# Performance work log

Measured on AMD Instinct MI355X. Metric: run time of the kernel, lower is better.

Reference implementation:

```python
import jax, jax.numpy as jnp
import numpy as np

B, S, H, W, C = 16, 32, 84, 84, 4
HID, NH, L, A = 256, 4, 2, 18
HD = HID // NH
THETA = 10000.0
EPS = 1e-6


def _ln(x, s, b):
    m = jnp.mean(x, axis=-1, keepdims=True)
    v = jnp.mean(jnp.square(x - m), axis=-1, keepdims=True)
    return (x - m) / jnp.sqrt(v + EPS) * s + b


def _conv(x, w):
    return jax.lax.conv_general_dilated(x, w, (1, 1), 'SAME', dimension_numbers=('NHWC', 'HWIO', 'NHWC'))


def _rotate_half(x):
    xe = x[..., ::2]
    xo = x[..., 1::2]
    return jnp.stack((-xo, xe), axis=-1).reshape(x.shape)


def _rope(q, k):
    d = q.shape[-1]
    pos = jnp.arange(q.shape[-2], dtype=jnp.float32)
    inv_freq = 1.0 / jnp.asarray(THETA, jnp.float32) ** (jnp.arange(0, d, 2, dtype=jnp.float32) / d)
    ang = pos[:, None] * inv_freq[None, :]
    sin = jnp.repeat(jnp.sin(ang), 2, axis=-1)[None, None].astype(q.dtype)
    cos = jnp.repeat(jnp.cos(ang), 2, axis=-1)[None, None].astype(q.dtype)
    return q * cos + _rotate_half(q) * sin, k * cos + _rotate_half(k) * sin


def setup_inputs() -> dict:
    key = jax.random.key(0)
    ks = jax.random.split(key, 20)
    he = lambda k, shp, fan: jax.random.normal(k, shp, jnp.float32) * np.sqrt(2.0 / fan)
    return {
        'x': jax.random.normal(ks[0], (B, S, H, W, C), jnp.float32),
        'attention_padding': jnp.ones((B, S), jnp.bool_),
        'conv0_w': he(ks[1], (3, 3, C, 32), 3 * 3 * C),
        'conv0_b': jnp.zeros((32,), jnp.float32),
        'ln_c0_s': jnp.ones((32,), jnp.float32), 'ln_c0_b': jnp.zeros((32,), jnp.float32),
        'conv1_w': he(ks[2], (3, 3, 32, 64), 3 * 3 * 32),
        'conv1_b': jnp.zeros((64,), jnp.float32),
        'ln_c1_s': jnp.ones((64,), jnp.float32), 'ln_c1_b': jnp.zeros((64,), jnp.float32),
        'proj_w': he(ks[3], (64, HID), 64), 'proj_b': jnp.zeros((HID,), jnp.float32),
        'ln_p_s': jnp.ones((HID,), jnp.float32), 'ln_p_b': jnp.zeros((HID,), jnp.float32),
        'attn_qkv_w': he(ks[4], (L, HID, 3 * HID), HID),
        'attn_qkv_b': jnp.zeros((L, 3 * HID), jnp.float32),
        'attn_out_w': he(ks[5], (L, HID, HID), HID),
        'attn_out_b': jnp.zeros((L, HID), jnp.float32),
        'ln_a_s': jnp.ones((L, HID), jnp.float32), 'ln_a_b': jnp.zeros((L, HID), jnp.float32),
        'up_w': he(ks[6], (L, HID, 2 * HID), HID),
        'down_w': he(ks[7], (L, 2 * HID, HID), 2 * HID),
        'ln_m_s': jnp.ones((L, HID), jnp.float32), 'ln_m_b': jnp.zeros((L, HID), jnp.float32),
        'head_w': he(ks[8], (HID, A), HID), 'head_b': jnp.zeros((A,), jnp.float32),
    }


def reference(x, attention_padding, conv0_w, conv0_b, ln_c0_s, ln_c0_b, conv1_w, conv1_b,
              ln_c1_s, ln_c1_b, proj_w, proj_b, ln_p_s, ln_p_b, attn_qkv_w, attn_qkv_b,
              attn_out_w, attn_out_b, ln_a_s, ln_a_b, up_w, down_w, ln_m_s, ln_m_b,
              head_w, head_b):
    b, s = x.shape[:2]
    # CNN feature extractor over flattened (B*S) frames
    h = x.reshape(b * s, *x.shape[2:])
    h = jax.nn.relu(_ln(_conv(h, conv0_w) + conv0_b, ln_c0_s, ln_c0_b))
    h = jax.nn.relu(_ln(_conv(h, conv1_w) + conv1_b, ln_c1_s, ln_c1_b))
    h = jnp.mean(h, axis=(1, 2)).reshape(b, s, -1)  # (B,S,64)
    h = _ln(h @ proj_w + proj_b, ln_p_s, ln_p_b)    # (B,S,HID)
    pad = attention_padding
    causal = jnp.tril(jnp.ones((s, s), jnp.bool_))
    mask = pad[:, None, None, :] & causal[None, None]
    scale = jnp.asarray(HD, h.dtype) ** (-0.5)
    neg = jnp.asarray(-1e9, h.dtype)
    for i in range(L):
        r = h
        qkv = h @ attn_qkv_w[i] + attn_qkv_b[i]
        q, k, v = jnp.split(qkv, 3, axis=-1)
        sh = lambda t: t.reshape(b, s, NH, HD).transpose(0, 2, 1, 3)
        q, k, v = sh(q), sh(k), sh(v)
        q, k = _rope(q, k)
        logits = jnp.einsum('bhqd,bhkd->bhqk', q, k) * scale
        attn = jax.nn.softmax(jnp.where(mask, logits, neg), axis=-1)
        y = jnp.einsum('bhqk,bhkd->bhqd', attn, v).transpose(0, 2, 1, 3).reshape(b, s, HID)
        y = (y @ attn_out_w[i] + attn_out_b[i]) * pad[:, :, None].astype(h.dtype)
        h = _ln(y, ln_a_s[i], ln_a_b[i]) + r
        r = h
        u = jax.nn.relu(h @ up_w[i])
        h = _ln(u @ down_w[i], ln_m_s[i], ln_m_b[i]) + r
    return h @ head_w + head_b  # (B,S,action_dim)
```

## Files before the change

kernel.cpp:

```cpp
#include <hip/hip_runtime.h>
#include <hip/hip_bf16.h>

#define LN_EPS 1e-6f

typedef __attribute__((ext_vector_type(8))) short bf16x8;
typedef __attribute__((ext_vector_type(4))) float fx4;

struct U8 { union { bf16x8 v; uint2 p[2]; }; };

__device__ __forceinline__ unsigned short f2bf(float f) {
    union { __hip_bfloat16 b; unsigned short u; } cv;
    cv.b = __float2bfloat16(f);
    return cv.u;
}

__global__ void k_pad(const unsigned char* __restrict__ p, float* __restrict__ padf) {
    __shared__ int cnt;
    int t = threadIdx.x;
    if (t == 0) cnt = 0;
    __syncthreads();
    if (p[t]) atomicAdd(&cnt, 1);
    __syncthreads();
    float v;
    if (cnt > 256) v = p[t] ? 1.f : 0.f;
    else           v = ((const int*)p)[t] ? 1.f : 0.f;
    padf[t] = v;
}

__global__ void k_wprep(const float* __restrict__ w1, const float* __restrict__ w0,
                        unsigned short* __restrict__ wtb) {
    int idx = blockIdx.x * 256 + threadIdx.x;
    if (idx < 18432) {
        int j  = idx & 7;
        int kg = (idx >> 3) & 3;
        int co = (idx >> 5) & 63;
        int tp = idx >> 11;
        wtb[idx] = f2bf(w1[((size_t)tp * 32 + kg * 8 + j) * 64 + co]);
    } else {
        int r = idx - 18432;
        int ch = r >> 6, k = r & 63;
        float v = 0.f;
        if (k < 36) v = w0[(size_t)k * 32 + ch];
        wtb[idx] = f2bf(v);
    }
}

__global__ void k_wpack(const float* __restrict__ qkvw, const float* __restrict__ ow,
                        const float* __restrict__ upw, const float* __restrict__ dww,
                        const float* __restrict__ pw, unsigned short* __restrict__ wpk)
{
    int idx = blockIdx.x * 256 + threadIdx.x;
    if (idx >= 1064960) return;
    float v;
    if (idx < 393216) {
        int l = idx / 196608, rm = idx % 196608, n = rm >> 8, k = rm & 255;
        v = qkvw[((size_t)l * 256 + k) * 768 + n];
    } else if (idx < 524288) {
        int r = idx - 393216, l = r >> 16, rm = r & 65535, n = rm >> 8, k = rm & 255;
        v = ow[((size_t)l * 256 + k) * 256 + n];
    } else if (idx < 786432) {
        int r = idx - 524288, l = r >> 17, rm = r & 131071, n = rm >> 8, k = rm & 255;
        v = upw[((size_t)l * 256 + k) * 512 + n];
    } else if (idx < 1048576) {
        int r = idx - 786432, l = r >> 17, rm = r & 131071, n = rm >> 9, k = rm & 511;
        v = dww[((size_t)l * 512 + k) * 256 + n];
    } else {
        int r = idx - 1048576, n = r >> 6, k = r & 63;
        v = pw[k * 256 + n];
    }
    wpk[idx] = f2bf(v);
}

__global__ __launch_bounds__(256, 3) void k_conv1(
    const float* __restrict__ x, const unsigned short* __restrict__ wtb,
    const float* __restrict__ c0b, const float* __restrict__ l0s, const float* __restrict__ l0b,
    const float* __restrict__ bias, const float* __restrict__ lns, const float* __restrict__ lnb,
    float* __restrict__ pooled)
{
    __shared__ __align__(16) unsigned short At[4][5][86][8];
    __shared__ __align__(16) unsigned short xs[7][86][4];
    __shared__ float pool_w[4][64];
    const int tid = threadIdx.x;
    const int img = blockIdx.x / 28;
    const int rg  = blockIdx.x - img * 28;
    const int y0  = rg * 3;

    const int lane = tid & 63;
    const int wv = tid >> 6;
    const int lo = lane & 15;
    const int kg = lane >> 4;

    if (tid >= 64 && tid < 104) {
        int z = tid - 64;
        int zk = z / 10, rem = z - zk * 10, zr = rem >> 1, side = rem & 1;
        *reinterpret_cast<uint4*>(&At[zk][zr][side ? 85 : 0][0]) = (uint4){0, 0, 0, 0};
    }
    if (tid >= 104 && tid < 118) {
        int z = tid - 104, row = z >> 1, side = z & 1;
        *reinterpret_cast<uint2*>(&xs[row][side ? 85 : 0][0]) = (uint2){0, 0};
    }
    for (int i = tid; i < 588; i += 256) {
        int row = i / 84, c = i - row * 84;
        int gy = y0 - 2 + row;
        float4 v = (float4){0.f, 0.f, 0.f, 0.f};
        if (gy >= 0 && gy < 84)
            v = *reinterpret_cast<const float4*>(x + ((size_t)img * 7056 + gy * 84 + c) * 4);
        unsigned l32 = (unsigned)f2bf(v.x) | ((unsigned)f2bf(v.y) << 16);
        unsigned h32 = (unsigned)f2bf(v.z) | ((unsigned)f2bf(v.w) << 16);
        *reinterpret_cast<uint2*>(&xs[row][c + 1][0]) = (uint2){l32, h32};
    }
    __syncthreads();

    {
        const unsigned short* wc0 = wtb + 18432;
        bf16x8 W0[2], W1[2];
        #pragma unroll
        for (int m = 0; m < 2; ++m) {
            W0[m] = *reinterpret_cast<const bf16x8*>(wc0 + (m * 16 + lo) * 64 + kg * 8);
            W1[m] = *reinterpret_cast<const bf16x8*>(wc0 + (m * 16 + lo) * 64 + 32 + kg * 8);
        }
        float cb[2][4], sg[2][4], bg[2][4];
        #pragma unroll
        for (int m = 0; m < 2; ++m)
            #pragma unroll
            for (int r = 0; r < 4; ++r) {
                int c = m * 16 + kg * 4 + r;
                cb[m][r] = c0b[c]; sg[m][r] = l0s[c]; bg[m][r] = l0b[c];
            }
        const int t0 = 2 * kg, t1 = 2 * kg + 1;
        const int dy0 = t0 / 3, dx0 = t0 % 3, dy1 = t1 / 3, dx1 = t1 % 3;
        const unsigned short* xsb = &xs[0][0][0];

        for (int it = 0; it < 7; ++it) {
            int np = it * 4 + wv;
            if (np >= 27) break;
            int px = np * 16 + lo;
            int pxc = px < 420 ? px : 419;
            int r5 = pxc / 84, col = pxc - r5 * 84;
            U8 a0u, a1u;
            a0u.p[0] = *reinterpret_cast<const uint2*>(xsb + ((r5 + dy0) * 86 + col + dx0) * 4);
            a0u.p[1] = *reinterpret_cast<const uint2*>(xsb + ((r5 + dy1) * 86 + col + dx1) * 4);
            if (kg == 0)
                a1u.p[0] = *reinterpret_cast<const uint2*>(xsb + ((r5 + 2) * 86 + col + 2) * 4);
            else
                a1u.p[0] = (uint2){0, 0};
            a1u.p[1] = (uint2){0, 0};

            fx4 c2[2];
            c2[0] = (fx4){0.f, 0.f, 0.f, 0.f};
            c2[1] = (fx4){0.f, 0.f, 0.f, 0.f};
            c2[0] = __builtin_amdgcn_mfma_f32_16x16x32_bf16(W0[0], a0u.v, c2[0], 0, 0, 0);
            c2[0] = __builtin_amdgcn_mfma_f32_16x16x32_bf16(W1[0], a1u.v, c2[0], 0, 0, 0);
            c2[1] = __builtin_amdgcn_mfma_f32_16x16x32_bf16(W0[1], a0u.v, c2[1], 0, 0, 0);
            c2[1] = __builtin_amdgcn_mfma_f32_16x16x32_bf16(W1[1], a1u.v, c2[1], 0, 0, 0);

            float v[2][4], s = 0.f, q = 0.f;
            #pragma unroll
            for (int m = 0; m < 2; ++m)
                #pragma unroll
                for (int r = 0; r < 4; ++r) {
                    v[m][r] = c2[m][r] + cb[m][r];
                    s += v[m][r]; q += v[m][r] * v[m][r];
                }
            s += __shfl_xor(s, 16); q += __shfl_xor(q, 16);
            s += __shfl_xor(s, 32); q += __shfl_xor(q, 32);
            float mn = s * (1.f / 32.f);
            float inv = rsqrtf(q * (1.f / 32.f) - mn * mn + LN_EPS);

            if (px < 420) {
                int yA = y0 - 1 + r5;
                bool gv = (unsigned)yA < 84u;
                #pragma unroll
                for (int m = 0; m < 2; ++m) {
                    uint2 pk = (uint2){0, 0};
                    if (gv) {
                        unsigned short o0 = f2bf(fmaxf((v[m][0] - mn) * inv * sg[m][0] + bg[m][0], 0.f));
                        unsigned short o1 = f2bf(fmaxf((v[m][1] - mn) * inv * sg[m][1] + bg[m][1], 0.f));
                        unsigned short o2 = f2bf(fmaxf((v[m][2] - mn) * inv * sg[m][2] + bg[m][2], 0.f));
                        unsigned short o3 = f2bf(fmaxf((v[m][3] - mn) * inv * sg[m][3] + bg[m][3], 0.f));
                        pk.x = (unsigned)o0 | ((unsigned)o1 << 16);
                        pk.y = (unsigned)o2 | ((unsigned)o3 << 16);
                    }
                    *reinterpret_cast<uint2*>(&At[2 * m + (kg >> 1)][r5][col + 1][(kg & 1) * 4]) = pk;
                }
            }
        }
    }
    __syncthreads();

    int abase[4];
    #pragma unroll
    for (int m = 0; m < 4; ++m) {
        int pl = wv * 64 + m * 16 + lo;
        if (pl > 251) pl = 251;
        int rl = pl / 84;
        int c = pl - rl * 84;
        abase[m] = ((kg * 5 + rl) * 86 + c) * 8;
    }

    fx4 acc[4][4];
    #pragma unroll
    for (int m = 0; m < 4; ++m)
        #pragma unroll
        for (int n = 0; n < 4; ++n) acc[m][n] = (fx4){0.f, 0.f, 0.f, 0.f};

    const unsigned short* Abase = &At[0][0][0][0];
    #pragma unroll
    for (int dy = 0; dy < 3; ++dy) {
        #pragma unroll
        for (int dx = 0; dx < 3; ++dx) {
            const int t = dy * 3 + dx;
            bf16x8 Bf[4];
            #pragma unroll
            for (int n = 0; n < 4; ++n)
                Bf[n] = *reinterpret_cast<const bf16x8*>(
                    wtb + (size_t)((t * 64 + n * 16 + lo) * 4 + kg) * 8);
            #pragma unroll
            for (int m = 0; m < 4; ++m) {
                bf16x8 Af = *reinterpret_cast<const bf16x8*>(Abase + abase[m] + (dy * 86 + dx) * 8);
                #pragma unroll
                for (int n = 0; n < 4; ++n)
                    acc[m][n] = __builtin_amdgcn_mfma_f32_16x16x32_bf16(Af, Bf[n], acc[m][n], 0, 0, 0);
            }
        }
    }

    float bs[4], ss[4], bb[4];
    #pragma unroll
    for (int n = 0; n < 4; ++n) {
        int c = n * 16 + lo;
        bs[n] = bias[c]; ss[n] = lns[c]; bb[n] = lnb[c];
    }
    float pv[4] = {0.f, 0.f, 0.f, 0.f};
    #pragma unroll
    for (int m = 0; m < 4; ++m) {
        #pragma unroll
        for (int r = 0; r < 4; ++r) {
            float v0 = acc[m][0][r] + bs[0], v1 = acc[m][1][r] + bs[1];
            float v2 = acc[m][2][r] + bs[2], v3 = acc[m][3][r] + bs[3];
            float s = v0 + v1 + v2 + v3;
            float q = v0 * v0 + v1 * v1 + v2 * v2 + v3 * v3;
            #pragma unroll
            for (int off = 1; off < 16; off <<= 1) {
                s += __shfl_xor(s, off);
                q += __shfl_xor(q, off);
            }
            float mn = s * (1.f / 64.f);
            float var = q * (1.f / 64.f) - mn * mn;
            float inv = rsqrtf(var + LN_EPS);
            int pix = wv * 64 + m * 16 + kg * 4 + r;
            float valid = (pix < 252) ? 1.f : 0.f;
            pv[0] += fmaxf((v0 - mn) * inv * ss[0] + bb[0], 0.f) * valid;
            pv[1] += fmaxf((v1 - mn) * inv * ss[1] + bb[1], 0.f) * valid;
            pv[2] += fmaxf((v2 - mn) * inv * ss[2] + bb[2], 0.f) * valid;
            pv[3] += fmaxf((v3 - mn) * inv * ss[3] + bb[3], 0.f) * valid;
        }
    }
    #pragma unroll
    for (int n = 0; n < 4; ++n) {
        float v = pv[n];
        v += __shfl_xor(v, 16);
        v += __shfl_xor(v, 32);
        if (lane < 16) pool_w[wv][n * 16 + lane] = v;
    }
    __syncthreads();
    if (tid < 64) {
        float s = pool_w[0][tid] + pool_w[1][tid] + pool_w[2][tid] + pool_w[3][tid];
        atomicAdd(&pooled[img * 64 + tid], s);
    }
}

template<int MT, int NT, int KS>
__device__ __forceinline__ void mfma_gemm(
    const unsigned short* A, int lda, int m0,
    const unsigned short* B, int ldb, int nt0,
    fx4 (&acc)[MT][NT], int lane)
{
    const int lo = lane & 15, kg = lane >> 4;
    #pragma unroll
    for (int ks = 0; ks < KS; ++ks) {
        const int k = ks * 32 + kg * 8;
        bf16x8 af[MT];
        #pragma unroll
        for (int m = 0; m < MT; ++m)
            af[m] = *reinterpret_cast<const bf16x8*>(A + (size_t)((m0 + m) * 16 + lo) * lda + k);
        #pragma unroll
        for (int n = 0; n < NT; ++n) {
            bf16x8 bf = *reinterpret_cast<const bf16x8*>(B + (size_t)((nt0 + n) * 16 + lo) * ldb + k);
            #pragma unroll
            for (int m = 0; m < MT; ++m)
                acc[m][n] = __builtin_amdgcn_mfma_f32_16x16x32_bf16(af[m], bf, acc[m][n], 0, 0, 0);
        }
    }
}

__device__ __forceinline__ void ln_update(
    const float* outs , float* hs, unsigned short* hs_b,
    const float* gs, const float* gb, bool resid, int w, int lane)
{
    #pragma unroll
    for (int i = 0; i < 4; ++i) {
        int r = w * 4 + i;
        float x[4], s = 0.f, q = 0.f;
        #pragma unroll
        for (int j = 0; j < 4; ++j) {
            x[j] = outs[r * 257 + lane + 64 * j];
            s += x[j]; q += x[j] * x[j];
        }
        #pragma unroll
        for (int off = 1; off < 64; off <<= 1) {
            s += __shfl_xor(s, off);
            q += __shfl_xor(q, off);
        }
        float mn = s * (1.f / 256.f);
        float inv = rsqrtf(q * (1.f / 256.f) - mn * mn + LN_EPS);
        #pragma unroll
        for (int j = 0; j < 4; ++j) {
            int c = lane + 64 * j;
            float nv = (x[j] - mn) * inv * gs[c] + gb[c];
            if (resid) nv += hs[r * 256 + c];
            hs[r * 256 + c] = nv;
            hs_b[r * 264 + c] = f2bf(nv);
        }
    }
}

__global__ __launch_bounds__(512) void k_xformer(
    const float* __restrict__ pooled, const float* __restrict__ padf,
    const unsigned short* __restrict__ wpk,
    const float* __restrict__ pb, const float* __restrict__ lps, const float* __restrict__ lpb,
    const float* __restrict__ qkvb, const float* __restrict__ obv,
    const float* __restrict__ las, const float* __restrict__ lab,
    const float* __restrict__ lms, const float* __restrict__ lmb,
    const float* __restrict__ hw, const float* __restrict__ hb,
    float* __restrict__ out)
{
    __shared__ __align__(16) char smem[124032];
    float* hs = (float*)(smem);
    unsigned short* hs_b = (unsigned short*)(smem + 32768);
    unsigned short* R1 = (unsigned short*)(smem + 49664);
    unsigned short* q_s = R1;
    unsigned short* k_s = R1 + 9216;
    unsigned short* us_b = R1;
    unsigned short* v_cm = (unsigned short*)(smem + 86528);
    unsigned short* ys_b = (unsigned short*)(smem + 107008);
    float* outs = (float*)(smem + 86528);
    unsigned short* pool_b = (unsigned short*)(smem + 86528);
    float* padc = (float*)(smem + 123904);

    const int b = blockIdx.x, t = threadIdx.x;
    const int w = t >> 6, lane = t & 63, lo = lane & 15, kg = lane >> 4;

    if (t < 32) padc[t] = padf[b * 32 + t];
    for (int i = t; i < 2048; i += 512) {
        int r = i >> 6, k = i & 63;
        pool_b[r * 72 + k] = f2bf(pooled[((size_t)b * 32 + r) * 64 + k] * (1.f / 7056.f));
    }
    __syncthreads();

    {
        fx4 acc[1][4];
        #pragma unroll
        for (int n = 0; n < 4; ++n) acc[0][n] = (fx4){0.f, 0.f, 0.f, 0.f};
        int m0 = w & 1, nt0 = (w >> 1) * 4;
        mfma_gemm<1, 4, 2>(pool_b, 72, m0, wpk + 1048576, 64, nt0, acc, lane);
        __syncthreads();
        #pragma unroll
        for (int n = 0; n < 4; ++n) {
            int c = (nt0 + n) * 16 + lo;
            float bias = pb[c];
            #pragma unroll
            for (int rg = 0; rg < 4; ++rg)
                outs[(m0 * 16 + kg * 4 + rg) * 257 + c] = acc[0][n][rg] + bias;
        }
        __syncthreads();
        ln_update(outs, hs, hs_b, lps, lpb, false, w, lane);
        __syncthreads();
    }

    for (int l = 0; l < 2; ++l) {
        const unsigned short* wq = wpk + (size_t)l * 196608;
        const unsigned short* wo = wpk + 393216 + (size_t)l * 65536;
        const unsigned short* wu = wpk + 524288 + (size_t)l * 131072;
        const unsigned short* wd = wpk + 786432 + (size_t)l * 131072;

        {
            fx4 acc[2][6];
            #pragma unroll
            for (int m = 0; m < 2; ++m)
                #pragma unroll
                for (int n = 0; n < 6; ++n) acc[m][n] = (fx4){0.f, 0.f, 0.f, 0.f};
            int nt0 = w * 6;
            mfma_gemm<2, 6, 8>(hs_b, 264, 0, wq, 256, nt0, acc, lane);
            #pragma unroll
            for (int n = 0; n < 6; ++n) {
                int c = (nt0 + n) * 16 + lo;
                int kind = c >> 8, cl = c & 255, h = cl >> 6, d = cl & 63;
                float bias = qkvb[l * 768 + c];
                if (kind < 2) {
                    int j = d >> 1;
                    float freq = exp2f(-(float)j * 0.41524101186f);
                    unsigned short* dst = (kind ? k_s : q_s) + h * 2304;
                    #pragma unroll
                    for (int m = 0; m < 2; ++m)
                        #pragma unroll
                        for (int rg = 0; rg < 4; ++rg) {
                            float val = acc[m][n][rg] + bias;
                            float prt = __shfl_xor(val, 1);
                            int r = m * 16 + kg * 4 + rg;
                            float sn, cs;
                            __sincosf((float)r * freq, &sn, &cs);
                            float rv = (d & 1) ? (val * cs + prt * sn) : (val * cs - prt * sn);
                            dst[r * 72 + d] = f2bf(rv);
                        }
                } else {
                    #pragma unroll
                    for (int m = 0; m < 2; ++m)
                        #pragma unroll
                        for (int rg = 0; rg < 4; ++rg) {
                            int r = m * 16 + kg * 4 + rg;
                            v_cm[(h * 64 + d) * 40 + r] = f2bf(acc[m][n][rg] + bias);
                        }
                }
            }
            __syncthreads();
        }

        {
            int h = w >> 1, mt = w & 1;
            fx4 sc[1][2];
            sc[0][0] = (fx4){0.f, 0.f, 0.f, 0.f};
            sc[0][1] = (fx4){0.f, 0.f, 0.f, 0.f};
            mfma_gemm<1, 2, 2>(q_s + h * 2304, 72, mt, k_s + h * 2304, 72, 0, sc, lane);
            __syncthreads();
            unsigned short* pa = R1 + h * 2304;
            float pad0 = padc[lo], pad1 = padc[16 + lo];
            #pragma unroll
            for (int rg = 0; rg < 4; ++rg) {
                int qr = mt * 16 + kg * 4 + rg;
                float v0 = (lo <= qr && pad0 != 0.f) ? sc[0][0][rg] * 0.125f : -1e9f;
                float v1 = ((16 + lo) <= qr && pad1 != 0.f) ? sc[0][1][rg] * 0.125f : -1e9f;
                float mx = fmaxf(v0, v1);
                #pragma unroll
                for (int off = 1; off < 16; off <<= 1) mx = fmaxf(mx, __shfl_xor(mx, off));
                float e0 = __expf(v0 - mx), e1 = __expf(v1 - mx);
                float sm = e0 + e1;
                #pragma unroll
                for (int off = 1; off < 16; off <<= 1) sm += __shfl_xor(sm, off);
                float inv = 1.f / sm;
                pa[qr * 40 + lo] = f2bf(e0 * inv);
                pa[qr * 40 + 16 + lo] = f2bf(e1 * inv);
            }
            __syncthreads();
        }

        {
            int h = w >> 1, mt = w & 1;
            fx4 yv[1][4];
            #pragma unroll
            for (int n = 0; n < 4; ++n) yv[0][n] = (fx4){0.f, 0.f, 0.f, 0.f};
            mfma_gemm<1, 4, 1>(R1 + h * 2304, 40, mt, v_cm + h * 2560, 40, 0, yv, lane);
            #pragma unroll
            for (int n = 0; n < 4; ++n) {
                int d = n * 16 + lo;
                #pragma unroll
                for (int rg = 0; rg < 4; ++rg)
                    ys_b[(mt * 16 + kg * 4 + rg) * 264 + h * 64 + d] = f2bf(yv[0][n][rg]);
            }
            __syncthreads();
        }

        {
            fx4 ac[2][2];
            #pragma unroll
            for (int m = 0; m < 2; ++m) { ac[m][0] = (fx4){0.f,0.f,0.f,0.f}; ac[m][1] = (fx4){0.f,0.f,0.f,0.f}; }
            mfma_gemm<2, 2, 8>(ys_b, 264, 0, wo, 256, w * 2, ac, lane);
            __syncthreads();
            #pragma unroll
            for (int n = 0; n < 2; ++n) {
                int c = (w * 2 + n) * 16 + lo;
                float bias = obv[l * 256 + c];
                #pragma unroll
                for (int m = 0; m < 2; ++m)
                    #pragma unroll
                    for (int rg = 0; rg < 4; ++rg) {
                        int r = m * 16 + kg * 4 + rg;
                        outs[r * 257 + c] = (ac[m][n][rg] + bias) * padc[r];
                    }
            }
            __syncthreads();
            ln_update(outs, hs, hs_b, las + l * 256, lab + l * 256, true, w, lane);
            __syncthreads();
        }

        {
            fx4 au[2][4];
            #pragma unroll
            for (int m = 0; m < 2; ++m)
                #pragma unroll
                for (int n = 0; n < 4; ++n) au[m][n] = (fx4){0.f, 0.f, 0.f, 0.f};
            mfma_gemm<2, 4, 8>(hs_b, 264, 0, wu, 256, w * 4, au, lane);
            #pragma unroll
            for (int n = 0; n < 4; ++n) {
                int c = (w * 4 + n) * 16 + lo;
                #pragma unroll
                for (int m = 0; m < 2; ++m)
                    #pragma unroll
                    for (int rg = 0; rg < 4; ++rg)
                        us_b[(m * 16 + kg * 4 + rg) * 520 + c] = f2bf(fmaxf(au[m][n][rg], 0.f));
            }
            __syncthreads();
        }

        {
            fx4 ad[2][2];
            #pragma unroll
            for (int m = 0; m < 2; ++m) { ad[m][0] = (fx4){0.f,0.f,0.f,0.f}; ad[m][1] = (fx4){0.f,0.f,0.f,0.f}; }
            mfma_gemm<2, 2, 16>(us_b, 520, 0, wd, 512, w * 2, ad, lane);
            #pragma unroll
            for (int n = 0; n < 2; ++n) {
                int c = (w * 2 + n) * 16 + lo;
                #pragma unroll
                for (int m = 0; m < 2; ++m)
                    #pragma unroll
                    for (int rg = 0; rg < 4; ++rg)
                        outs[(m * 16 + kg * 4 + rg) * 257 + c] = ad[m][n][rg];
            }
            __syncthreads();
            ln_update(outs, hs, hs_b, lms + l * 256, lmb + l * 256, true, w, lane);
            __syncthreads();
        }
    }

    for (int idx = t; idx < 576; idx += 512) {
        int r = idx / 18, a = idx - r * 18;
        float acch = hb[a];
        #pragma unroll 8
        for (int k = 0; k < 256; ++k) acch = fmaf(hs[r * 256 + k], hw[k * 18 + a], acch);
        out[((size_t)b * 32 + r) * 18 + a] = acch;
    }
}

extern "C" void kernel_launch(void* const* d_in, const int* in_sizes, int n_in,
                              void* d_out, int out_size, void* d_ws, size_t ws_size,
                              hipStream_t stream)
{
    (void)in_sizes; (void)n_in; (void)out_size; (void)ws_size;
    const float* x   = (const float*)d_in[0];
    const unsigned char* pad = (const unsigned char*)d_in[1];
    const float* c0w = (const float*)d_in[2];
    const float* c0b = (const float*)d_in[3];
    const float* l0s = (const float*)d_in[4];
    const float* l0b = (const float*)d_in[5];
    const float* c1w = (const float*)d_in[6];
    const float* c1b = (const float*)d_in[7];
    const float* l1s = (const float*)d_in[8];
    const float* l1b = (const float*)d_in[9];
    const float* pw  = (const float*)d_in[10];
    const float* pb  = (const float*)d_in[11];
    const float* lps = (const float*)d_in[12];
    const float* lpb = (const float*)d_in[13];
    const float* qkvw = (const float*)d_in[14];
    const float* qkvb = (const float*)d_in[15];
    const float* ow  = (const float*)d_in[16];
    const float* obv = (const float*)d_in[17];
    const float* las = (const float*)d_in[18];
    const float* lab = (const float*)d_in[19];
    const float* upw = (const float*)d_in[20];
    const float* dww = (const float*)d_in[21];
    const float* lms = (const float*)d_in[22];
    const float* lmb = (const float*)d_in[23];
    const float* hw  = (const float*)d_in[24];
    const float* hb  = (const float*)d_in[25];
    float* out = (float*)d_out;

    char* ws = (char*)d_ws;
    size_t off = 0;
    auto alloc = [&](size_t bytes) -> void* {
        void* p = ws + off;
        off = (off + bytes + 255) & ~(size_t)255;
        return p;
    };
    unsigned short* wtb = (unsigned short*)alloc(20480 * 2);
    unsigned short* wpk = (unsigned short*)alloc((size_t)1064960 * 2);
    float* pooled = (float*)alloc(512 * 64 * 4);
    float* padf   = (float*)alloc(512 * 4);

    hipMemsetAsync(pooled, 0, 512 * 64 * 4, stream);
    k_pad<<<1, 512, 0, stream>>>(pad, padf);
    k_wprep<<<80, 256, 0, stream>>>(c1w, c0w, wtb);
    k_wpack<<<4160, 256, 0, stream>>>(qkvw, ow, upw, dww, pw, wpk);
    k_conv1<<<14336, 256, 0, stream>>>(x, wtb, c0b, l0s, l0b, c1b, l1s, l1b, pooled);
    k_xformer<<<16, 512, 0, stream>>>(pooled, padf, wpk, pb, lps, lpb,
                                      qkvb, obv, las, lab, lms, lmb, hw, hb, out);
}
```

Before: 435.9 us.

## Transpose conv1 MFMA operands so channels map to rows; MFMA head GEMM

Swaps the MFMA operand roles in the conv1 kernel so weights form the A operand and pixels the B operand, putting channels along accumulator rows. The LayerNorm statistics then reduce with two cross-lane shuffles per pixel group instead of four per element, and bias, scale and shift load as float4. The final action head moves from a scalar FMA loop over fp32 weights to a bf16 MFMA GEMM using a new zero-padded packed weight block. The head now runs in bf16, which adds rounding error, and the epilogue keeps 16 pooled partials per lane that need extra shuffles.

```diff
diff --git a/kernel.cpp b/kernel.cpp
--- a/kernel.cpp
+++ b/kernel.cpp
@@ -47,10 +47,11 @@
 
 __global__ void k_wpack(const float* __restrict__ qkvw, const float* __restrict__ ow,
                         const float* __restrict__ upw, const float* __restrict__ dww,
-                        const float* __restrict__ pw, unsigned short* __restrict__ wpk)
+                        const float* __restrict__ pw, const float* __restrict__ hw,
+                        unsigned short* __restrict__ wpk)
 {
     int idx = blockIdx.x * 256 + threadIdx.x;
-    if (idx >= 1064960) return;
+    if (idx >= 1073152) return;
     float v;
     if (idx < 393216) {
         int l = idx / 196608, rm = idx % 196608, n = rm >> 8, k = rm & 255;
@@ -64,9 +65,12 @@
     } else if (idx < 1048576) {
         int r = idx - 786432, l = r >> 17, rm = r & 131071, n = rm >> 9, k = rm & 511;
         v = dww[((size_t)l * 512 + k) * 256 + n];
-    } else {
+    } else if (idx < 1064960) {
         int r = idx - 1048576, n = r >> 6, k = r & 63;
         v = pw[k * 256 + n];
+    } else {
+        int r = idx - 1064960, n = r >> 8, k = r & 255;
+        v = (n < 18) ? hw[(size_t)k * 18 + n] : 0.f;
     }
     wpk[idx] = f2bf(v);
 }
@@ -79,7 +83,7 @@
 {
     __shared__ __align__(16) unsigned short At[4][5][86][8];
     __shared__ __align__(16) unsigned short xs[7][86][4];
-    __shared__ float pool_w[4][64];
+    __shared__ __align__(16) float pool_w[4][64];
     const int tid = threadIdx.x;
     const int img = blockIdx.x / 28;
     const int rg  = blockIdx.x - img * 28;
@@ -190,12 +194,12 @@
 
     int abase[4];
     #pragma unroll
-    for (int m = 0; m < 4; ++m) {
-        int pl = wv * 64 + m * 16 + lo;
+    for (int n = 0; n < 4; ++n) {
+        int pl = wv * 64 + n * 16 + lo;
         if (pl > 251) pl = 251;
         int rl = pl / 84;
         int c = pl - rl * 84;
-        abase[m] = ((kg * 5 + rl) * 86 + c) * 8;
+        abase[n] = ((kg * 5 + rl) * 86 + c) * 8;
     }
 
     fx4 acc[4][4];
@@ -210,58 +214,71 @@
         #pragma unroll
         for (int dx = 0; dx < 3; ++dx) {
             const int t = dy * 3 + dx;
-            bf16x8 Bf[4];
-            #pragma unroll
-            for (int n = 0; n < 4; ++n)
-                Bf[n] = *reinterpret_cast<const bf16x8*>(
-                    wtb + (size_t)((t * 64 + n * 16 + lo) * 4 + kg) * 8);
-            #pragma unroll
-            for (int m = 0; m < 4; ++m) {
-                bf16x8 Af = *reinterpret_cast<const bf16x8*>(Abase + abase[m] + (dy * 86 + dx) * 8);
-                #pragma unroll
-                for (int n = 0; n < 4; ++n)
-                    acc[m][n] = __builtin_amdgcn_mfma_f32_16x16x32_bf16(Af, Bf[n], acc[m][n], 0, 0, 0);
-            }
-        }
-    }
-
-    float bs[4], ss[4], bb[4];
+            bf16x8 Wf[4];
+            #pragma unroll
+            for (int m = 0; m < 4; ++m)
+                Wf[m] = *reinterpret_cast<const bf16x8*>(
+                    wtb + (size_t)((t * 64 + m * 16 + lo) * 4 + kg) * 8);
+            #pragma unroll
+            for (int n = 0; n < 4; ++n) {
+                bf16x8 Pf = *reinterpret_cast<const bf16x8*>(Abase + abase[n] + (dy * 86 + dx) * 8);
+                #pragma unroll
+                for (int m = 0; m < 4; ++m)
+                    acc[m][n] = __builtin_amdgcn_mfma_f32_16x16x32_bf16(Wf[m], Pf, acc[m][n], 0, 0, 0);
+            }
+        }
+    }
+
+    float s4[4] = {0.f, 0.f, 0.f, 0.f}, q4[4] = {0.f, 0.f, 0.f, 0.f};
+    #pragma unroll
+    for (int m = 0; m < 4; ++m) {
+        float4 cbv = *reinterpret_cast<const float4*>(bias + m * 16 + kg * 4);
+        #pragma unroll
+        for (int n = 0; n < 4; ++n)
+            #pragma unroll
+            for (int r = 0; r < 4; ++r) {
+                float val = acc[m][n][r] + (&cbv.x)[r];
+                acc[m][n][r] = val;
+                s4[n] += val; q4[n] += val * val;
+            }
+    }
+    float mn4[4], iv4[4], pval[4];
     #pragma unroll
     for (int n = 0; n < 4; ++n) {
-        int c = n * 16 + lo;
-        bs[n] = bias[c]; ss[n] = lns[c]; bb[n] = lnb[c];
-    }
-    float pv[4] = {0.f, 0.f, 0.f, 0.f};
+        float s = s4[n], q = q4[n];
+        s += __shfl_xor(s, 16); q += __shfl_xor(q, 16);
+        s += __shfl_xor(s, 32); q += __shfl_xor(q, 32);
+        float mn = s * (1.f / 64.f);
+        mn4[n] = mn;
+        iv4[n] = rsqrtf(q * (1.f / 64.f) - mn * mn + LN_EPS);
+        pval[n] = (wv * 64 + n * 16 + lo < 252) ? 1.f : 0.f;
+    }
+    float pool[4][4] = {{0.f}};
     #pragma unroll
     for (int m = 0; m < 4; ++m) {
-        #pragma unroll
-        for (int r = 0; r < 4; ++r) {
-            float v0 = acc[m][0][r] + bs[0], v1 = acc[m][1][r] + bs[1];
-            float v2 = acc[m][2][r] + bs[2], v3 = acc[m][3][r] + bs[3];
-            float s = v0 + v1 + v2 + v3;
-            float q = v0 * v0 + v1 * v1 + v2 * v2 + v3 * v3;
-            #pragma unroll
-            for (int off = 1; off < 16; off <<= 1) {
-                s += __shfl_xor(s, off);
-                q += __shfl_xor(q, off);
-            }
-            float mn = s * (1.f / 64.f);
-            float var = q * (1.f / 64.f) - mn * mn;
-            float inv = rsqrtf(var + LN_EPS);
-            int pix = wv * 64 + m * 16 + kg * 4 + r;
-            float valid = (pix < 252) ? 1.f : 0.f;
-            pv[0] += fmaxf((v0 - mn) * inv * ss[0] + bb[0], 0.f) * valid;
-            pv[1] += fmaxf((v1 - mn) * inv * ss[1] + bb[1], 0.f) * valid;
-            pv[2] += fmaxf((v2 - mn) * inv * ss[2] + bb[2], 0.f) * valid;
-            pv[3] += fmaxf((v3 - mn) * inv * ss[3] + bb[3], 0.f) * valid;
-        }
-    }
-    #pragma unroll
-    for (int n = 0; n < 4; ++n) {
-        float v = pv[n];
-        v += __shfl_xor(v, 16);
-        v += __shfl_xor(v, 32);
-        if (lane < 16) pool_w[wv][n * 16 + lane] = v;
+        float4 sgv = *reinterpret_cast<const float4*>(lns + m * 16 + kg * 4);
+        float4 bgv = *reinterpret_cast<const float4*>(lnb + m * 16 + kg * 4);
+        #pragma unroll
+        for (int n = 0; n < 4; ++n)
+            #pragma unroll
+            for (int r = 0; r < 4; ++r) {
+                float o = fmaxf((acc[m][n][r] - mn4[n]) * iv4[n] * (&sgv.x)[r] + (&bgv.x)[r], 0.f);
+                pool[m][r] = fmaf(o, pval[n], pool[m][r]);
+            }
+    }
+    #pragma unroll
+    for (int off = 1; off < 16; off <<= 1)
+        #pragma unroll
+        for (int m = 0; m < 4; ++m)
+            #pragma unroll
+            for (int r = 0; r < 4; ++r)
+                pool[m][r] += __shfl_xor(pool[m][r], off);
+    if (lo == 0) {
+        #pragma unroll
+        for (int m = 0; m < 4; ++m) {
+            float4 pk = (float4){pool[m][0], pool[m][1], pool[m][2], pool[m][3]};
+            *reinterpret_cast<float4*>(&pool_w[wv][m * 16 + kg * 4]) = pk;
+        }
     }
     __syncthreads();
     if (tid < 64) {
@@ -332,8 +349,7 @@
     const float* __restrict__ qkvb, const float* __restrict__ obv,
     const float* __restrict__ las, const float* __restrict__ lab,
     const float* __restrict__ lms, const float* __restrict__ lmb,
-    const float* __restrict__ hw, const float* __restrict__ hb,
-    float* __restrict__ out)
+    const float* __restrict__ hb, float* __restrict__ out)
 {
     __shared__ __align__(16) char smem[124032];
     float* hs = (float*)(smem);
@@ -532,12 +548,18 @@
         }
     }
 
-    for (int idx = t; idx < 576; idx += 512) {
-        int r = idx / 18, a = idx - r * 18;
-        float acch = hb[a];
-        #pragma unroll 8
-        for (int k = 0; k < 256; ++k) acch = fmaf(hs[r * 256 + k], hw[k * 18 + a], acch);
-        out[((size_t)b * 32 + r) * 18 + a] = acch;
+    if (w < 4) {
+        int mt = w >> 1, nt = w & 1;
+        fx4 hd[1][1];
+        hd[0][0] = (fx4){0.f, 0.f, 0.f, 0.f};
+        mfma_gemm<1, 1, 8>(hs_b, 264, mt, wpk + 1064960, 256, nt, hd, lane);
+        int cc = nt * 16 + lo;
+        if (cc < 18) {
+            float bias = hb[cc];
+            #pragma unroll
+            for (int rg = 0; rg < 4; ++rg)
+                out[((size_t)b * 32 + mt * 16 + kg * 4 + rg) * 18 + cc] = hd[0][0][rg] + bias;
+        }
     }
 }
 
@@ -582,15 +604,15 @@
         return p;
     };
     unsigned short* wtb = (unsigned short*)alloc(20480 * 2);
-    unsigned short* wpk = (unsigned short*)alloc((size_t)1064960 * 2);
+    unsigned short* wpk = (unsigned short*)alloc((size_t)1073152 * 2);
     float* pooled = (float*)alloc(512 * 64 * 4);
     float* padf   = (float*)alloc(512 * 4);
 
     hipMemsetAsync(pooled, 0, 512 * 64 * 4, stream);
     k_pad<<<1, 512, 0, stream>>>(pad, padf);
     k_wprep<<<80, 256, 0, stream>>>(c1w, c0w, wtb);
-    k_wpack<<<4160, 256, 0, stream>>>(qkvw, ow, upw, dww, pw, wpk);
+    k_wpack<<<4192, 256, 0, stream>>>(qkvw, ow, upw, dww, pw, hw, wpk);
     k_conv1<<<14336, 256, 0, stream>>>(x, wtb, c0b, l0s, l0b, c1b, l1s, l1b, pooled);
     k_xformer<<<16, 512, 0, stream>>>(pooled, padf, wpk, pb, lps, lpb,
-                                      qkvb, obv, las, lab, lms, lmb, hw, hb, out);
-}
+                                      qkvb, obv, las, lab, lms, lmb, hb, out);
+}
```

After: 407.0 us. -6.6%, faster.
